# Optimization experiments

Hardware: AMD Instinct MI355X
Metric: run time of the kernel (lower is better)

Reference implementation:

```python
import jax, jax.numpy as jnp
import numpy as np

N_EMBED = 288
HEAD_SIZE = 32


def setup_inputs() -> dict:
    key = jax.random.key(0)
    kx, kk, kq, kv = jax.random.split(key, 4)
    B, T, C = 16, 2048, N_EMBED
    scale = 1.0 / np.sqrt(C)
    return {
        "x": jax.random.normal(kx, (B, T, C), dtype=jnp.float32),
        # Linear(n_embed, head_size, bias=False) weights, stored as [C, head_size]
        "Wk": jax.random.normal(kk, (C, HEAD_SIZE), dtype=jnp.float32) * scale,
        "Wq": jax.random.normal(kq, (C, HEAD_SIZE), dtype=jnp.float32) * scale,
        "Wv": jax.random.normal(kv, (C, HEAD_SIZE), dtype=jnp.float32) * scale,
    }


def reference(x, Wk, Wq, Wv):
    # x: [B, T, C]
    k = x @ Wk  # [B, T, hs]
    q = x @ Wq
    v = x @ Wv
    # NOTE: source computes k @ q^T (not q @ k^T) -- reproduce faithfully.
    weights = jnp.einsum("bth,bsh->bts", k, q) * (HEAD_SIZE ** -0.5)  # [B, T, T]
    T = x.shape[1]
    causal = jnp.tril(jnp.ones((T, T), dtype=bool))
    weights = jnp.where(causal, weights, -jnp.inf)
    weights = jax.nn.softmax(weights, axis=-1)
    return weights @ v  # [B, T, hs]
```

## Files before the change

kernel.cpp:

```cpp
#include <hip/hip_runtime.h>

typedef __bf16 bf16;
typedef __attribute__((ext_vector_type(8))) __bf16 bf16x8;
typedef __attribute__((ext_vector_type(4))) float f32x4;

#define BATCH 16
#define SEQ   2048
#define CEMB  288
#define HS    32
#define NROWS (BATCH * SEQ)

#define XSTR 296

__global__ __launch_bounds__(384, 3) void proj_kernel(
    const float* __restrict__ x, const float* __restrict__ Wk,
    const float* __restrict__ Wq, const float* __restrict__ Wv,
    bf16* __restrict__ Kx, bf16* __restrict__ Qm, bf16* __restrict__ VT)
{
    __shared__ __align__(16) bf16 Xl[32 * XSTR];

    const int tid  = threadIdx.x;
    const int wv   = tid >> 6;
    const int lane = tid & 63;
    const int quad = lane >> 4;
    const int ln   = lane & 15;
    const int dsel = wv >> 1;
    const int half = wv & 1;

    const float SCALE = 0.25519486439582695f;

    const float* Wsrc = (dsel == 0) ? Wk : ((dsel == 1) ? Wq : Wv);
    const float mul = (dsel == 0) ? SCALE : 1.0f;
    bf16x8 wfrag[9];
    for (int kc = 0; kc < 9; ++kc) {
        bf16x8 f;
#pragma unroll
        for (int j = 0; j < 8; ++j) {
            float w = Wsrc[(kc * 32 + quad * 8 + j) * HS + half * 16 + ln];
            f[j] = (bf16)(w * mul);
        }
        wfrag[kc] = f;
    }

    const int wgRowBase = blockIdx.x * 64;
    for (int it = 0; it < 2; ++it) {
        __syncthreads();
        const int rb = wgRowBase + it * 32;
#pragma unroll
        for (int i = 0; i < 6; ++i) {
            int f = tid + 384 * i;
            int row = f / 72;
            int c4  = f - row * 72;
            f32x4 v = ((const f32x4*)x)[(rb + row) * 72 + c4];
            bf16* d = &Xl[row * XSTR + c4 * 4];
            d[0] = (bf16)v[0]; d[1] = (bf16)v[1];
            d[2] = (bf16)v[2]; d[3] = (bf16)v[3];
        }
        __syncthreads();

#pragma unroll
        for (int m = 0; m < 2; ++m) {
            f32x4 acc = {0.f, 0.f, 0.f, 0.f};
#pragma unroll
            for (int kc = 0; kc < 9; ++kc) {
                bf16x8 a = *(const bf16x8*)&Xl[(m * 16 + ln) * XSTR + kc * 32 + quad * 8];
                acc = __builtin_amdgcn_mfma_f32_16x16x32_bf16(a, wfrag[kc], acc, 0, 0, 0);
            }
#pragma unroll
            for (int reg = 0; reg < 4; ++reg) {
                int gr = rb + m * 16 + quad * 4 + reg;
                bf16 val = (bf16)acc[reg];
                if (dsel == 0) {
                    Kx[gr * HS + half * 16 + ln] = val;
                } else if (dsel == 1) {
                    Qm[gr * HS + half * 16 + ln] = val;
                } else {
                    VT[(gr >> 11) * (HS * SEQ) + (half * 16 + ln) * SEQ + (gr & 2047)] = val;
                }
            }
        }
    }
}


__constant__ unsigned char MAP_TILE[72] = {
    15,15,15,15,15,15,15,
    14,14,14,14,14,14,14,
    13,13,13,13,13,13,
    12,12,12,12,12,12,
    11,11,11,11,11,
    10,10,10,10,10,
    9,9,9,9,
    8,8,8,8,
    7,7,7,
    6,6,6,
    5,5,
    4,4,
    3,
    2,
    15,13,11,9,7,5,3,1,
    14,12,10,8,6,4,2,0 };
__constant__ unsigned char MAP_CHUNK[72] = {
    0,1,2,3,4,5,6,
    0,1,2,3,4,5,6,
    0,1,2,3,4,5,
    0,1,2,3,4,5,
    0,1,2,3,4,
    0,1,2,3,4,
    0,1,2,3,
    0,1,2,3,
    0,1,2,
    0,1,2,
    0,1,
    0,1,
    0,
    0,
    7,6,5,4,3,2,1,0,
    7,6,5,4,3,2,1,0 };

__global__ __launch_bounds__(256, 4) void attn_kernel(
    const bf16* __restrict__ Kx, const bf16* __restrict__ Qm,
    const bf16* __restrict__ VT,
    float* __restrict__ Opart, float* __restrict__ Lpart)
{
    const int tid  = threadIdx.x;
    const int w    = tid >> 6;
    const int lane = tid & 63;
    const int quad = lane >> 4;
    const int ln   = lane & 15;

    const int bid   = blockIdx.x;
    const int u     = bid >> 4;
    const int b     = ((bid & 7) << 1) | ((bid >> 3) & 1);
    const int tile  = MAP_TILE[u];
    const int chunk = MAP_CHUNK[u];
    const int t0    = tile * 128;
    const int cs    = chunk * 256;
    const int ce    = min(cs + 256, t0 + 128);

    const bf16* Kb = Kx + b * SEQ * HS;
    const bf16* Qb = Qm + b * SEQ * HS;
    const bf16* Vb = VT + b * HS * SEQ;

    int tsub[2];
    bf16x8 kfrag[2];
#pragma unroll
    for (int m = 0; m < 2; ++m) {
        tsub[m] = t0 + w * 32 + m * 16;
        kfrag[m] = *(const bf16x8*)&Kb[(tsub[m] + ln) * HS + quad * 8];
    }

    const int qrow = 8 * (ln >> 2) + (ln & 3);
    const int t_row = ln;

    f32x4 Of[2][2] = {};
    float Lacc[2]  = {0.f, 0.f};

    for (int s0 = cs; s0 < ce; s0 += 64) {
        if (s0 >= tsub[1] + 16) break;

        bf16x8 qfA[2], qfB[2];
#pragma unroll
        for (int c = 0; c < 2; ++c) {
            qfA[c] = *(const bf16x8*)&Qb[(s0 + 32 * c + qrow) * HS + quad * 8];
            qfB[c] = *(const bf16x8*)&Qb[(s0 + 32 * c + qrow + 4) * HS + quad * 8];
        }
        bf16x8 vf[2][2];
#pragma unroll
        for (int hb = 0; hb < 2; ++hb)
#pragma unroll
            for (int c = 0; c < 2; ++c)
                vf[hb][c] = *(const bf16x8*)&Vb[(hb * 16 + ln) * SEQ + s0 + c * 32 + quad * 8];

#pragma unroll
        for (int m = 0; m < 2; ++m) {
            const int t = tsub[m] + t_row;
#pragma unroll
            for (int c = 0; c < 2; ++c) {
                const int sb = s0 + 32 * c;
                if (sb >= tsub[m] + 16) continue;
                const bool diag = (sb + 31 > tsub[m]);

                f32x4 z = {0.f, 0.f, 0.f, 0.f};
                f32x4 SA = __builtin_amdgcn_mfma_f32_16x16x32_bf16(qfA[c], kfrag[m], z, 0, 0, 0);
                f32x4 SB = __builtin_amdgcn_mfma_f32_16x16x32_bf16(qfB[c], kfrag[m], z, 0, 0, 0);

                const int sAb = sb + 8 * quad;
                float pA[4], pB[4];
#pragma unroll
                for (int r = 0; r < 4; ++r) {
                    pA[r] = __builtin_amdgcn_exp2f(SA[r]);
                    pB[r] = __builtin_amdgcn_exp2f(SB[r]);
                    if (diag) {
                        pA[r] = (sAb + r     <= t) ? pA[r] : 0.0f;
                        pB[r] = (sAb + r + 4 <= t) ? pB[r] : 0.0f;
                    }
                    Lacc[m] += pA[r] + pB[r];
                }

                bf16x8 ap;
#pragma unroll
                for (int r = 0; r < 4; ++r) {
                    ap[r]     = (bf16)pA[r];
                    ap[r + 4] = (bf16)pB[r];
                }

                Of[m][0] = __builtin_amdgcn_mfma_f32_16x16x32_bf16(ap, vf[0][c], Of[m][0], 0, 0, 0);
                Of[m][1] = __builtin_amdgcn_mfma_f32_16x16x32_bf16(ap, vf[1][c], Of[m][1], 0, 0, 0);
            }
        }
    }

#pragma unroll
    for (int m = 0; m < 2; ++m) {
        if (cs >= tsub[m] + 16) continue;
#pragma unroll
        for (int reg = 0; reg < 4; ++reg) {
            int gr = b * SEQ + tsub[m] + quad * 4 + reg;
            float* od = Opart + ((size_t)chunk * NROWS + gr) * HS;
            od[ln]      = Of[m][0][reg];
            od[16 + ln] = Of[m][1][reg];
        }
        float l = Lacc[m];
        l += __shfl_xor(l, 16, 64);
        l += __shfl_xor(l, 32, 64);
        if (quad == 0)
            Lpart[chunk * NROWS + b * SEQ + tsub[m] + ln] = l;
    }
}

__global__ __launch_bounds__(256) void combine_kernel(
    const float* __restrict__ Opart, const float* __restrict__ Lpart,
    float* __restrict__ out)
{
    int idx = blockIdx.x * 256 + threadIdx.x;
    int gr = idx >> 3, h4 = idx & 7;
    int t  = gr & 2047;
    int nc = (t >> 8) + 1;
    f32x4 acc = {0.f, 0.f, 0.f, 0.f};
    float l = 0.f;
    for (int c = 0; c < nc; ++c) {
        acc += ((const f32x4*)Opart)[((size_t)c * NROWS + gr) * 8 + h4];
        l   += Lpart[c * NROWS + gr];
    }
    f32x4 r = acc / l;
    ((f32x4*)out)[idx] = r;
}

extern "C" void kernel_launch(void* const* d_in, const int* in_sizes, int n_in,
                              void* d_out, int out_size, void* d_ws, size_t ws_size,
                              hipStream_t stream) {
    (void)in_sizes; (void)n_in; (void)out_size; (void)ws_size;
    const float* x  = (const float*)d_in[0];
    const float* Wk = (const float*)d_in[1];
    const float* Wq = (const float*)d_in[2];
    const float* Wv = (const float*)d_in[3];

    char* ws = (char*)d_ws;
    bf16*  Kx    = (bf16*)(ws);
    bf16*  Qm    = (bf16*)(ws + 2097152);
    bf16*  VT    = (bf16*)(ws + 4194304);
    float* Opart = (float*)(ws + 6291456);
    float* Lpart = (float*)(ws + 6291456 + 33554432);
    float* out   = (float*)d_out;

    hipLaunchKernelGGL(proj_kernel, dim3(512), dim3(384), 0, stream,
                       x, Wk, Wq, Wv, Kx, Qm, VT);
    hipLaunchKernelGGL(attn_kernel, dim3(1152), dim3(256), 0, stream,
                       Kx, Qm, VT, Opart, Lpart);
    hipLaunchKernelGGL(combine_kernel, dim3(1024), dim3(256), 0, stream,
                       Opart, Lpart, out);
}
```

Before: 107.7 us.

## Use 512-wide key chunks and compute softmax row sums with an MFMA against ones

The causal split-K chunk width doubles from 256 to 512. The work map shrinks to 40 units per batch, giving a 640-block grid, and the combine kernel has fewer partials to read and sum. Row-sum accumulation moves from scalar adds plus cross-lane shuffles to an extra MFMA of the probability fragment against a vector of ones. This uses the bf16-rounded probabilities in the denominator, matching the values fed into the numerator. The trade-off is less parallelism and longer per-block loops, which may leave the GPU under-occupied or poorly load-balanced.

```diff
diff --git a/kernel.cpp b/kernel.cpp
--- a/kernel.cpp
+++ b/kernel.cpp
@@ -83,40 +83,12 @@
 }
 
 
-__constant__ unsigned char MAP_TILE[72] = {
-    15,15,15,15,15,15,15,
-    14,14,14,14,14,14,14,
-    13,13,13,13,13,13,
-    12,12,12,12,12,12,
-    11,11,11,11,11,
-    10,10,10,10,10,
-    9,9,9,9,
-    8,8,8,8,
-    7,7,7,
-    6,6,6,
-    5,5,
-    4,4,
-    3,
-    2,
-    15,13,11,9,7,5,3,1,
-    14,12,10,8,6,4,2,0 };
-__constant__ unsigned char MAP_CHUNK[72] = {
-    0,1,2,3,4,5,6,
-    0,1,2,3,4,5,6,
-    0,1,2,3,4,5,
-    0,1,2,3,4,5,
-    0,1,2,3,4,
-    0,1,2,3,4,
-    0,1,2,3,
-    0,1,2,3,
-    0,1,2,
-    0,1,2,
-    0,1,
-    0,1,
-    0,
-    0,
-    7,6,5,4,3,2,1,0,
-    7,6,5,4,3,2,1,0 };
+__constant__ unsigned char MAP_TILE[40] = {
+    4,5,6,7, 8,8,9,9, 10,10,11,11, 12,12,12, 13,13,13, 14,14,14, 15,15,15,
+    3,7,11,15, 2,6,10,14, 1,5,9,13, 0,4,8,12 };
+__constant__ unsigned char MAP_CHUNK[40] = {
+    0,0,0,0, 0,1,0,1, 0,1,0,1, 0,1,2, 0,1,2, 0,1,2, 0,1,2,
+    0,1,2,3, 0,1,2,3, 0,1,2,3, 0,1,2,3 };
 
 __global__ __launch_bounds__(256, 4) void attn_kernel(
     const bf16* __restrict__ Kx, const bf16* __restrict__ Qm,
@@ -135,8 +107,8 @@
     const int tile  = MAP_TILE[u];
     const int chunk = MAP_CHUNK[u];
     const int t0    = tile * 128;
-    const int cs    = chunk * 256;
-    const int ce    = min(cs + 256, t0 + 128);
+    const int cs    = chunk * 512;
+    const int ce    = min(cs + 512, t0 + 128);
 
     const bf16* Kb = Kx + b * SEQ * HS;
     const bf16* Qb = Qm + b * SEQ * HS;
@@ -149,12 +121,15 @@
         tsub[m] = t0 + w * 32 + m * 16;
         kfrag[m] = *(const bf16x8*)&Kb[(tsub[m] + ln) * HS + quad * 8];
     }
+    bf16x8 ones;
+#pragma unroll
+    for (int j = 0; j < 8; ++j) ones[j] = (bf16)1.0f;
 
     const int qrow = 8 * (ln >> 2) + (ln & 3);
     const int t_row = ln;
 
     f32x4 Of[2][2] = {};
-    float Lacc[2]  = {0.f, 0.f};
+    f32x4 Lf[2]    = {};
 
     for (int s0 = cs; s0 < ce; s0 += 64) {
         if (s0 >= tsub[1] + 16) break;
@@ -195,7 +170,6 @@
                         pA[r] = (sAb + r     <= t) ? pA[r] : 0.0f;
                         pB[r] = (sAb + r + 4 <= t) ? pB[r] : 0.0f;
                     }
-                    Lacc[m] += pA[r] + pB[r];
                 }
 
                 bf16x8 ap;
@@ -207,6 +181,7 @@
 
                 Of[m][0] = __builtin_amdgcn_mfma_f32_16x16x32_bf16(ap, vf[0][c], Of[m][0], 0, 0, 0);
                 Of[m][1] = __builtin_amdgcn_mfma_f32_16x16x32_bf16(ap, vf[1][c], Of[m][1], 0, 0, 0);
+                Lf[m]    = __builtin_amdgcn_mfma_f32_16x16x32_bf16(ap, ones,    Lf[m],    0, 0, 0);
             }
         }
     }
@@ -220,12 +195,8 @@
             float* od = Opart + ((size_t)chunk * NROWS + gr) * HS;
             od[ln]      = Of[m][0][reg];
             od[16 + ln] = Of[m][1][reg];
-        }
-        float l = Lacc[m];
-        l += __shfl_xor(l, 16, 64);
-        l += __shfl_xor(l, 32, 64);
-        if (quad == 0)
-            Lpart[chunk * NROWS + b * SEQ + tsub[m] + ln] = l;
+            if (ln == 0) Lpart[chunk * NROWS + gr] = Lf[m][reg];
+        }
     }
 }
 
@@ -236,7 +207,7 @@
     int idx = blockIdx.x * 256 + threadIdx.x;
     int gr = idx >> 3, h4 = idx & 7;
     int t  = gr & 2047;
-    int nc = (t >> 8) + 1;
+    int nc = (t >> 9) + 1;
     f32x4 acc = {0.f, 0.f, 0.f, 0.f};
     float l = 0.f;
     for (int c = 0; c < nc; ++c) {
@@ -261,12 +232,12 @@
     bf16*  Qm    = (bf16*)(ws + 2097152);
     bf16*  VT    = (bf16*)(ws + 4194304);
     float* Opart = (float*)(ws + 6291456);
-    float* Lpart = (float*)(ws + 6291456 + 33554432);
+    float* Lpart = (float*)(ws + 6291456 + 16777216);
     float* out   = (float*)d_out;
 
     hipLaunchKernelGGL(proj_kernel, dim3(512), dim3(384), 0, stream,
                        x, Wk, Wq, Wv, Kx, Qm, VT);
-    hipLaunchKernelGGL(attn_kernel, dim3(1152), dim3(256), 0, stream,
+    hipLaunchKernelGGL(attn_kernel, dim3(640), dim3(256), 0, stream,
                        Kx, Qm, VT, Opart, Lpart);
     hipLaunchKernelGGL(combine_kernel, dim3(1024), dim3(256), 0, stream,
                        Opart, Lpart, out);
```

New measurement: 105.1 us. -2.4%, faster.
